# Optimization experiments

Measured on AMD Instinct MI355X. Metric: run time of the kernel, lower is better.

Reference implementation:

```python
import jax, jax.numpy as jnp
import numpy as np

EPS = 1e-5

def _layernorm(x, gamma, beta):
    mu = x.mean(-1, keepdims=True)
    var = ((x - mu) ** 2).mean(-1, keepdims=True)
    return (x - mu) * jax.lax.rsqrt(var + EPS) * gamma + beta

def setup_inputs() -> dict:
    key = jax.random.key(0)
    k1, k2, k3, k4, k5 = jax.random.split(key, 5)
    V, P, IN, H, OUT = 200000, 32, 4, 16, 16
    B, GH, GW, GZ = 1, 512, 512, 32
    features = jax.random.normal(k1, (V, P, IN), dtype=jnp.float32)
    num_points = jax.random.randint(k2, (V,), 1, P + 1, dtype=jnp.int32)
    # unique voxel coordinates: distinct linear indices decomposed into (b,ix,iy,iz)
    total = B * GH * GW * GZ
    stride = total // V  # >=1, so arange(V)*stride are distinct and in-range
    lin = jnp.arange(V, dtype=jnp.int32) * stride
    iz = lin % GZ
    iy = (lin // GZ) % GW
    ix = (lin // (GZ * GW)) % GH
    b = lin // (GZ * GW * GH)
    coords = jnp.stack([b, ix, iy, iz], axis=1).astype(jnp.int32)
    # parameters (kaiming-ish small init)
    W1 = jax.random.normal(k3, (IN, H), dtype=jnp.float32) * 0.5
    b1 = jnp.zeros((H,), jnp.float32)
    g1 = jnp.ones((H,), jnp.float32)
    be1 = jnp.zeros((H,), jnp.float32)
    W2 = jax.random.normal(k4, (H, OUT), dtype=jnp.float32) * 0.25
    b2 = jnp.zeros((OUT,), jnp.float32)
    g2 = jnp.ones((OUT,), jnp.float32)
    be2 = jnp.zeros((OUT,), jnp.float32)
    return {"features": features, "num_points": num_points, "coords": coords,
            "W1": W1, "b1": b1, "g1": g1, "be1": be1,
            "W2": W2, "b2": b2, "g2": g2, "be2": be2,
            "batch_size": B, "grid_h": GH, "grid_w": GW, "grid_z": GZ}

def reference(features, num_points, coords, W1, b1, g1, be1, W2, b2, g2, be2,
              batch_size, grid_h, grid_w, grid_z):
    V, P, _ = features.shape
    mask = (jnp.arange(P)[None, :] < num_points[:, None]).astype(features.dtype)  # (V,P)
    h = _layernorm(features @ W1 + b1, g1, be1)          # (V,P,H)
    h = jax.nn.relu(h)
    x = h @ W2 + b2                                      # (V,P,OUT)
    x = (x * mask[:, :, None]).sum(axis=1)               # masked sum pool -> (V,OUT)
    x = _layernorm(x, g2, be2)                           # (V,OUT)
    dense = jnp.zeros((batch_size, grid_h, grid_w, grid_z, x.shape[-1]), x.dtype)
    bi, ix, iy, iz = coords[:, 0], coords[:, 1], coords[:, 2], coords[:, 3]
    return dense.at[bi, ix, iy, iz].set(x, mode="drop")
```

## Files before the change

### kernel.cpp

```cpp
#include <hip/hip_runtime.h>


#define TPB 256

__global__ void __launch_bounds__(TPB)
voxel_pointnet_kernel(
    const float* __restrict__ features,
    const int* __restrict__ num_points,
    const int* __restrict__ coords,
    const float* __restrict__ W1, const float* __restrict__ b1,
    const float* __restrict__ g1, const float* __restrict__ be1,
    const float* __restrict__ W2, const float* __restrict__ b2,
    const float* __restrict__ g2, const float* __restrict__ be2,
    const int* __restrict__ pB, const int* __restrict__ pGH,
    const int* __restrict__ pGW, const int* __restrict__ pGZ,
    float* __restrict__ out, int V, int P)
{
    __shared__ float sW1[64], sb1[16], sg1[16], sbe1[16];
    __shared__ float sW2[256], sb2[16], sg2[16], sbe2[16];
    int t = threadIdx.x;
    if (t < 64)  sW1[t] = W1[t];
    if (t < 256) sW2[t] = W2[t];
    if (t < 16) {
        sb1[t] = b1[t]; sg1[t] = g1[t]; sbe1[t] = be1[t];
        sb2[t] = b2[t]; sg2[t] = g2[t]; sbe2[t] = be2[t];
    }
    __syncthreads();

    int g = blockIdx.x * TPB + t;
    int v = g >> 2;
    int q = g & 3;
    if (v >= V) return;

    int np = num_points[v];
    np = np < 0 ? 0 : (np > P ? P : np);

    float hsum[16];
    #pragma unroll
    for (int j = 0; j < 16; j++) hsum[j] = 0.f;

    const float4* fp = (const float4*)features + (size_t)v * 32 + q * 8;

    #pragma unroll
    for (int i = 0; i < 8; i++) {
        float4 f = fp[i];
        int p = q * 8 + i;
        float h[16];
        float mu = 0.f;
        #pragma unroll
        for (int j = 0; j < 16; j++) {
            float acc = sb1[j];
            acc = fmaf(f.x, sW1[j],      acc);
            acc = fmaf(f.y, sW1[16 + j], acc);
            acc = fmaf(f.z, sW1[32 + j], acc);
            acc = fmaf(f.w, sW1[48 + j], acc);
            h[j] = acc;
            mu += acc;
        }
        mu *= 0.0625f;
        float var = 0.f;
        #pragma unroll
        for (int j = 0; j < 16; j++) { float d = h[j] - mu; var = fmaf(d, d, var); }
        var *= 0.0625f;
        float r = rsqrtf(var + 1e-5f);
        float keep = (p < np) ? 1.f : 0.f;
        #pragma unroll
        for (int j = 0; j < 16; j++) {
            float val = fmaf((h[j] - mu) * r, sg1[j], sbe1[j]);
            hsum[j] += keep * fmaxf(val, 0.f);
        }
    }

    #pragma unroll
    for (int j = 0; j < 16; j++) hsum[j] += __shfl_xor(hsum[j], 1, 64);
    #pragma unroll
    for (int j = 0; j < 16; j++) hsum[j] += __shfl_xor(hsum[j], 2, 64);

    if (q != 0) return;

    float fn = (float)np;
    float x[16];
    float mu = 0.f;
    #pragma unroll
    for (int j = 0; j < 16; j++) {
        float acc = fn * sb2[j];
        #pragma unroll
        for (int kk = 0; kk < 16; kk++) acc = fmaf(hsum[kk], sW2[kk * 16 + j], acc);
        x[j] = acc;
        mu += acc;
    }
    mu *= 0.0625f;
    float var = 0.f;
    #pragma unroll
    for (int j = 0; j < 16; j++) { float d = x[j] - mu; var = fmaf(d, d, var); }
    var *= 0.0625f;
    float r = rsqrtf(var + 1e-5f);
    #pragma unroll
    for (int j = 0; j < 16; j++) x[j] = fmaf((x[j] - mu) * r, sg2[j], sbe2[j]);

    int B = *pB, GH = *pGH, GW = *pGW, GZ = *pGZ;
    int4 c = *(const int4*)(coords + (size_t)v * 4);
    if ((unsigned)c.x >= (unsigned)B || (unsigned)c.y >= (unsigned)GH ||
        (unsigned)c.z >= (unsigned)GW || (unsigned)c.w >= (unsigned)GZ) return;

    size_t o = ((((size_t)c.x * GH + c.y) * GW + c.z) * GZ + c.w) * 16;
    float4* op = (float4*)(out + o);
    op[0] = make_float4(x[0],  x[1],  x[2],  x[3]);
    op[1] = make_float4(x[4],  x[5],  x[6],  x[7]);
    op[2] = make_float4(x[8],  x[9],  x[10], x[11]);
    op[3] = make_float4(x[12], x[13], x[14], x[15]);
}

extern "C" void kernel_launch(void* const* d_in, const int* in_sizes, int n_in,
                              void* d_out, int out_size, void* d_ws, size_t ws_size,
                              hipStream_t stream) {
    const float* features = (const float*)d_in[0];
    const int*   num_points = (const int*)d_in[1];
    const int*   coords   = (const int*)d_in[2];
    const float* W1  = (const float*)d_in[3];
    const float* b1  = (const float*)d_in[4];
    const float* g1  = (const float*)d_in[5];
    const float* be1 = (const float*)d_in[6];
    const float* W2  = (const float*)d_in[7];
    const float* b2  = (const float*)d_in[8];
    const float* g2  = (const float*)d_in[9];
    const float* be2 = (const float*)d_in[10];
    const int* pB  = (const int*)d_in[11];
    const int* pGH = (const int*)d_in[12];
    const int* pGW = (const int*)d_in[13];
    const int* pGZ = (const int*)d_in[14];
    float* out = (float*)d_out;

    int V  = in_sizes[1];
    int IN = in_sizes[3] / in_sizes[4];
    int P  = in_sizes[0] / (V * IN);


    long long threads = (long long)V * 4;
    int blocks = (int)((threads + TPB - 1) / TPB);
    voxel_pointnet_kernel<<<blocks, TPB, 0, stream>>>(
        features, num_points, coords, W1, b1, g1, be1, W2, b2, g2, be2,
        pB, pGH, pGW, pGZ, out, V, P);
}
```

Measured before the change: 593.9 us.

## Assign one voxel per thread and hold layer-1 weights in registers

Each voxel now gets one thread that loops over all 32 points, where before four threads shared a voxel and combined partial sums with cross-lane shuffles. The first-layer weights, bias, gamma and beta are loaded into registers instead of LDS, and launch bounds ask for two blocks per CU. This removes the shuffle reduction, the idle lanes in the epilogue and the LDS reads in the inner loop. In exchange there are 4x fewer threads, feature reads are no longer coalesced across lanes (each thread strides through 512 bytes), and register pressure rises.

```diff
diff --git a/kernel.cpp b/kernel.cpp
--- a/kernel.cpp
+++ b/kernel.cpp
@@ -3,7 +3,7 @@
 
 #define TPB 256
 
-__global__ void __launch_bounds__(TPB)
+__global__ void __launch_bounds__(TPB, 2)
 voxel_pointnet_kernel(
     const float* __restrict__ features,
     const int* __restrict__ num_points,
@@ -16,20 +16,30 @@
     const int* __restrict__ pGW, const int* __restrict__ pGZ,
     float* __restrict__ out, int V, int P)
 {
-    __shared__ float sW1[64], sb1[16], sg1[16], sbe1[16];
     __shared__ float sW2[256], sb2[16], sg2[16], sbe2[16];
     int t = threadIdx.x;
-    if (t < 64)  sW1[t] = W1[t];
     if (t < 256) sW2[t] = W2[t];
-    if (t < 16) {
-        sb1[t] = b1[t]; sg1[t] = g1[t]; sbe1[t] = be1[t];
-        sb2[t] = b2[t]; sg2[t] = g2[t]; sbe2[t] = be2[t];
-    }
+    if (t < 16) { sb2[t] = b2[t]; sg2[t] = g2[t]; sbe2[t] = be2[t]; }
     __syncthreads();
 
-    int g = blockIdx.x * TPB + t;
-    int v = g >> 2;
-    int q = g & 3;
+    float w1[64];
+    #pragma unroll
+    for (int i = 0; i < 16; i++) {
+        float4 t4 = ((const float4*)W1)[i];
+        w1[i*4+0] = t4.x; w1[i*4+1] = t4.y; w1[i*4+2] = t4.z; w1[i*4+3] = t4.w;
+    }
+    float vb1[16], vg1[16], vbe1[16];
+    #pragma unroll
+    for (int i = 0; i < 4; i++) {
+        float4 a = ((const float4*)b1)[i];
+        vb1[i*4+0] = a.x; vb1[i*4+1] = a.y; vb1[i*4+2] = a.z; vb1[i*4+3] = a.w;
+        float4 b = ((const float4*)g1)[i];
+        vg1[i*4+0] = b.x; vg1[i*4+1] = b.y; vg1[i*4+2] = b.z; vg1[i*4+3] = b.w;
+        float4 c = ((const float4*)be1)[i];
+        vbe1[i*4+0] = c.x; vbe1[i*4+1] = c.y; vbe1[i*4+2] = c.z; vbe1[i*4+3] = c.w;
+    }
+
+    int v = blockIdx.x * TPB + t;
     if (v >= V) return;
 
     int np = num_points[v];
@@ -39,21 +49,20 @@
     #pragma unroll
     for (int j = 0; j < 16; j++) hsum[j] = 0.f;
 
-    const float4* fp = (const float4*)features + (size_t)v * 32 + q * 8;
+    const float4* fp = (const float4*)features + (size_t)v * 32;
 
-    #pragma unroll
-    for (int i = 0; i < 8; i++) {
-        float4 f = fp[i];
-        int p = q * 8 + i;
+    #pragma unroll 4
+    for (int p = 0; p < 32; p++) {
+        float4 f = fp[p];
         float h[16];
         float mu = 0.f;
         #pragma unroll
         for (int j = 0; j < 16; j++) {
-            float acc = sb1[j];
-            acc = fmaf(f.x, sW1[j],      acc);
-            acc = fmaf(f.y, sW1[16 + j], acc);
-            acc = fmaf(f.z, sW1[32 + j], acc);
-            acc = fmaf(f.w, sW1[48 + j], acc);
+            float acc = vb1[j];
+            acc = fmaf(f.x, w1[j],      acc);
+            acc = fmaf(f.y, w1[16 + j], acc);
+            acc = fmaf(f.z, w1[32 + j], acc);
+            acc = fmaf(f.w, w1[48 + j], acc);
             h[j] = acc;
             mu += acc;
         }
@@ -66,17 +75,10 @@
         float keep = (p < np) ? 1.f : 0.f;
         #pragma unroll
         for (int j = 0; j < 16; j++) {
-            float val = fmaf((h[j] - mu) * r, sg1[j], sbe1[j]);
+            float val = fmaf((h[j] - mu) * r, vg1[j], vbe1[j]);
             hsum[j] += keep * fmaxf(val, 0.f);
         }
     }
-
-    #pragma unroll
-    for (int j = 0; j < 16; j++) hsum[j] += __shfl_xor(hsum[j], 1, 64);
-    #pragma unroll
-    for (int j = 0; j < 16; j++) hsum[j] += __shfl_xor(hsum[j], 2, 64);
-
-    if (q != 0) return;
 
     float fn = (float)np;
     float x[16];
@@ -136,8 +138,7 @@
     int P  = in_sizes[0] / (V * IN);
 
 
-    long long threads = (long long)V * 4;
-    int blocks = (int)((threads + TPB - 1) / TPB);
+    int blocks = (V + TPB - 1) / TPB;
     voxel_pointnet_kernel<<<blocks, TPB, 0, stream>>>(
         features, num_points, coords, W1, b1, g1, be1, W2, b2, g2, be2,
         pB, pGH, pGW, pGZ, out, V, P);
```

Measured after the change: 560.0 us. 5.7% less time.
